# Optimization experiments

Hardware: AMD Instinct MI355X
Metric: run time of the kernel (lower is better)

Reference implementation:

```python
import jax, jax.numpy as jnp
import numpy as np

N = 100000       # num nodes
E = 3200000      # num edges (avg degree 32)
F_IN = 128       # num_node_features
HID = 16         # hidden dim hard-coded in Net
C = 10           # num_classes


def setup_inputs() -> dict:
    key = jax.random.key(0)
    k1, k2, k3, k4 = jax.random.split(key, 4)
    x = jax.random.normal(k1, (N, F_IN), dtype=jnp.float32)
    edge_index = jax.random.randint(k2, (2, E), 0, N, dtype=jnp.int32)
    W1 = jax.random.normal(k3, (F_IN, HID), dtype=jnp.float32) * 0.05
    b1 = jnp.zeros((HID,), dtype=jnp.float32)
    W2 = jax.random.normal(k4, (HID, C), dtype=jnp.float32) * 0.05
    b2 = jnp.zeros((C,), dtype=jnp.float32)
    return {"x": x, "edge_index": edge_index, "W1": W1, "b1": b1, "W2": W2, "b2": b2}


def reference(x, edge_index, W1, b1, W2, b2):
    # GCNConv: out = D^{-1/2} (A + I) D^{-1/2} X W + b   (add self-loops)
    loops = jnp.arange(N, dtype=edge_index.dtype)
    row = jnp.concatenate([edge_index[0], loops])  # source nodes
    col = jnp.concatenate([edge_index[1], loops])  # target nodes

    # symmetric normalization (degrees include self-loops, so deg >= 1)
    deg = jax.ops.segment_sum(jnp.ones_like(col, dtype=jnp.float32), col, num_segments=N)
    dis = jax.lax.rsqrt(deg)
    norm = dis[row] * dis[col]  # [E+N]

    def gcn_conv(h, W, b):
        h = h @ W                               # [N, d_out] small GEMM first
        msg = h[row] * norm[:, None]            # gather + scale, [E+N, d_out]
        out = jax.ops.segment_sum(msg, col, num_segments=N)  # scatter-add
        return out + b

    h = jax.nn.relu(gcn_conv(x, W1, b1))
    # F.dropout(training=False) is identity in eval mode
    logits = gcn_conv(h, W2, b2)
    return jax.nn.log_softmax(logits, axis=1)
```

## Files before the change

kernel.cpp:

```cpp
#include <hip/hip_runtime.h>
#include <math.h>

#define N_NODES 100000
#define N_EDGES 3200000
#define F_IN 128
#define HID 16
#define C_OUT 10
#define WIN 256
#define NDIG 391
#define PNB2 500
#define EPB 6400
#define SCN (NDIG * PNB2)
#define SB1 764
#define MAXE3 10
#define CSRLDS 10240

typedef unsigned short u16;
typedef unsigned int u32;

__device__ __forceinline__ float bf2f(u16 u) {
    return __uint_as_float(((u32)u) << 16);
}
__device__ __forceinline__ u16 f2bf(float f) {
    u32 x = __float_as_uint(f);
    u32 r = (x + 0x7fffu + ((x >> 16) & 1u)) >> 16;
    return (u16)r;
}
__device__ __forceinline__ void acc8(float* a, uint4 w) {
    a[0] += bf2f((u16)(w.x & 0xffff)); a[1] += bf2f((u16)(w.x >> 16));
    a[2] += bf2f((u16)(w.y & 0xffff)); a[3] += bf2f((u16)(w.y >> 16));
    a[4] += bf2f((u16)(w.z & 0xffff)); a[5] += bf2f((u16)(w.z >> 16));
    a[6] += bf2f((u16)(w.w & 0xffff)); a[7] += bf2f((u16)(w.w >> 16));
}

__global__ void k_pcnt(const int* __restrict__ col, int* __restrict__ blkhistA) {
    __shared__ int h[NDIG];
    for (int i = threadIdx.x; i < NDIG; i += 256) h[i] = 0;
    __syncthreads();
    const uint4* c4 = (const uint4*)(col + blockIdx.x * EPB);
    for (int i = threadIdx.x; i < EPB / 4; i += 256) {
        uint4 c = c4[i];
        atomicAdd(&h[c.x >> 8], 1);
        atomicAdd(&h[c.y >> 8], 1);
        atomicAdd(&h[c.z >> 8], 1);
        atomicAdd(&h[c.w >> 8], 1);
    }
    __syncthreads();
    for (int d = threadIdx.x; d < NDIG; d += 256)
        blkhistA[d * PNB2 + blockIdx.x] = h[d];
}

__global__ void k_s1(const int* __restrict__ blkhistA, int* __restrict__ psum) {
    __shared__ int sm[256];
    int i = blockIdx.x * 256 + threadIdx.x;
    sm[threadIdx.x] = (i < SCN) ? blkhistA[i] : 0;
    __syncthreads();
    for (int off = 128; off > 0; off >>= 1) {
        if (threadIdx.x < off) sm[threadIdx.x] += sm[threadIdx.x + off];
        __syncthreads();
    }
    if (threadIdx.x == 0) psum[blockIdx.x] = sm[0];
}

__global__ void k_s3(const int* __restrict__ blkhistA, const int* __restrict__ psum,
                     int* __restrict__ blkhistB) {
    __shared__ int ps[1024];
    __shared__ int sm[256];
    int t = threadIdx.x;
    for (int i = t; i < 1024; i += 256) ps[i] = (i < SB1) ? psum[i] : 0;
    __syncthreads();
    for (int off = 1; off < 1024; off <<= 1) {
        int v[4];
#pragma unroll
        for (int j = 0; j < 4; j++) {
            int idx = t + j * 256;
            v[j] = ps[idx] + ((idx >= off) ? ps[idx - off] : 0);
        }
        __syncthreads();
#pragma unroll
        for (int j = 0; j < 4; j++) ps[t + j * 256] = v[j];
        __syncthreads();
    }
    int bpre = (blockIdx.x > 0) ? ps[blockIdx.x - 1] : 0;

    int i = blockIdx.x * 256 + t;
    int v = (i < SCN) ? blkhistA[i] : 0;
    sm[t] = v;
    __syncthreads();
    for (int off = 1; off < 256; off <<= 1) {
        int a = sm[t];
        int b = (t >= off) ? sm[t - off] : 0;
        __syncthreads();
        sm[t] = a + b;
        __syncthreads();
    }
    if (i < SCN) blkhistB[i] = bpre + sm[t] - v;
}

__global__ void __launch_bounds__(512) k_pwrite(
        const int* __restrict__ row, const int* __restrict__ col,
        const int* __restrict__ blkhistA, const int* __restrict__ blkhistB,
        u32* __restrict__ staging) {
    __shared__ u32 sorted[EPB];
    __shared__ u16 dwin[EPB];
    __shared__ int gbase[NDIG];
    __shared__ int lbase[NDIG];
    __shared__ int lcur[NDIG];
    __shared__ int scan[512];

    int t = threadIdx.x;
    int b = blockIdx.x;
    int hv = 0;
    if (t < NDIG) {
        hv = blkhistA[t * PNB2 + b];
        gbase[t] = blkhistB[t * PNB2 + b];
        lcur[t] = 0;
    }
    scan[t] = hv;
    __syncthreads();
    for (int off = 1; off < 512; off <<= 1) {
        int v = scan[t];
        int u = (t >= off) ? scan[t - off] : 0;
        __syncthreads();
        scan[t] = v + u;
        __syncthreads();
    }
    if (t < NDIG) lbase[t] = scan[t] - hv;
    __syncthreads();

    const uint4* c4 = (const uint4*)(col + b * EPB);
    const uint4* r4 = (const uint4*)(row + b * EPB);
    for (int i = t; i < EPB / 4; i += 512) {
        uint4 c = c4[i];
        uint4 r = r4[i];
        int d, rank, pos;
        d = (int)(c.x >> 8); rank = atomicAdd(&lcur[d], 1); pos = lbase[d] + rank;
        sorted[pos] = ((c.x & 255u) << 17) | r.x; dwin[pos] = (u16)d;
        d = (int)(c.y >> 8); rank = atomicAdd(&lcur[d], 1); pos = lbase[d] + rank;
        sorted[pos] = ((c.y & 255u) << 17) | r.y; dwin[pos] = (u16)d;
        d = (int)(c.z >> 8); rank = atomicAdd(&lcur[d], 1); pos = lbase[d] + rank;
        sorted[pos] = ((c.z & 255u) << 17) | r.z; dwin[pos] = (u16)d;
        d = (int)(c.w >> 8); rank = atomicAdd(&lcur[d], 1); pos = lbase[d] + rank;
        sorted[pos] = ((c.w & 255u) << 17) | r.w; dwin[pos] = (u16)d;
    }
    __syncthreads();

    for (int i = t; i < EPB; i += 512) {
        int d = dwin[i];
        staging[gbase[d] + (i - lbase[d])] = sorted[i];
    }
}

__global__ void __launch_bounds__(256) k_gemm1d(
        const float* __restrict__ x, const float* __restrict__ W1,
        const u32* __restrict__ staging, const int* __restrict__ blkhistB,
        float* __restrict__ dis, u16* __restrict__ h1s) {
    __shared__ float Ws[F_IN * HID];
    __shared__ int cnt[WIN];
    int w = blockIdx.x;
    int t = threadIdx.x;
    for (int i = t; i < F_IN * HID; i += 256) Ws[i] = W1[i];
    cnt[t] = 0;
    __syncthreads();
    int start = blkhistB[w * PNB2];
    int end = (w == NDIG - 1) ? N_EDGES : blkhistB[(w + 1) * PNB2];
    for (int i = start + t; i < end; i += 256)
        atomicAdd(&cnt[staging[i] >> 17], 1);
    __syncthreads();

    int node = w * WIN + t;
    if (node >= N_NODES) return;
    float d = rsqrtf(1.0f + (float)cnt[t]);
    dis[node] = d;

    float acc[HID];
#pragma unroll
    for (int j = 0; j < HID; j++) acc[j] = 0.f;

    const float4* xr = (const float4*)(x + (size_t)node * F_IN);
#pragma unroll 2
    for (int k4 = 0; k4 < F_IN / 4; k4++) {
        float4 v = xr[k4];
        float xv[4] = {v.x, v.y, v.z, v.w};
#pragma unroll
        for (int kk = 0; kk < 4; kk++) {
            const float4* wr = (const float4*)(Ws + (k4 * 4 + kk) * HID);
            float4 w0 = wr[0], w1 = wr[1], w2 = wr[2], w3 = wr[3];
            float xs = xv[kk];
            acc[0]  += xs * w0.x; acc[1]  += xs * w0.y; acc[2]  += xs * w0.z; acc[3]  += xs * w0.w;
            acc[4]  += xs * w1.x; acc[5]  += xs * w1.y; acc[6]  += xs * w1.z; acc[7]  += xs * w1.w;
            acc[8]  += xs * w2.x; acc[9]  += xs * w2.y; acc[10] += xs * w2.z; acc[11] += xs * w2.w;
            acc[12] += xs * w3.x; acc[13] += xs * w3.y; acc[14] += xs * w3.z; acc[15] += xs * w3.w;
        }
    }

    u32 p[8];
#pragma unroll
    for (int i = 0; i < 8; i++)
        p[i] = (u32)f2bf(acc[2 * i] * d) | ((u32)f2bf(acc[2 * i + 1] * d) << 16);
    u32* dst = (u32*)(h1s + (size_t)node * HID);
#pragma unroll
    for (int i = 0; i < 8; i++) dst[i] = p[i];
}

__global__ void __launch_bounds__(1024) k_gl1f(
        u32* staging, const int* __restrict__ blkhistB,
        const u16* __restrict__ h1s, const float* __restrict__ b1,
        const float* __restrict__ W2,
        int* __restrict__ offs, u16* __restrict__ h2s) {
    __shared__ u32 sorted[CSRLDS];
    __shared__ int cnt[WIN];
    __shared__ int sbase[WIN];
    __shared__ int cur[WIN];
    __shared__ float Ws[HID * C_OUT];
    __shared__ float b1s[HID];
    int w = blockIdx.x;
    int t = threadIdx.x;
    if (t < HID * C_OUT) Ws[t] = W2[t];
    if (t < HID) b1s[t] = b1[t];
    if (t < WIN) cnt[t] = 0;
    __syncthreads();
    int start = blkhistB[w * PNB2];
    int end = (w == NDIG - 1) ? N_EDGES : blkhistB[(w + 1) * PNB2];
    int m = end - start;
    u32 buf[MAXE3];
    int n = 0;
#pragma unroll
    for (int k = 0; k < MAXE3; k++) {
        int i = k * 1024 + t;
        if (i < m) {
            u32 e = staging[start + i];
            buf[k] = e;
            n = k + 1;
            atomicAdd(&cnt[e >> 17], 1);
        }
    }
    __syncthreads();
    if (t < WIN) sbase[t] = cnt[t];
    __syncthreads();
    for (int off = 1; off < WIN; off <<= 1) {
        int v = 0;
        if (t < WIN) {
            v = sbase[t];
            if (t >= off) v += sbase[t - off];
        }
        __syncthreads();
        if (t < WIN) sbase[t] = v;
        __syncthreads();
    }
    if (t < WIN) {
        int excl = sbase[t] - cnt[t];
        sbase[t] = excl;
        cur[t] = excl;
        int node = w * WIN + t;
        if (node < N_NODES) offs[node] = start + excl;
    }
    if (w == 0 && t == 0) offs[N_NODES] = N_EDGES;
    __syncthreads();
#pragma unroll
    for (int k = 0; k < MAXE3; k++) {
        if (k < n) {
            u32 e = buf[k];
            int pos = atomicAdd(&cur[(int)(e >> 17)], 1);
            sorted[pos] = e;
        }
    }
    __syncthreads();
    for (int i = t; i < m; i += 1024)
        staging[start + i] = sorted[i];

    const uint4* hb = (const uint4*)h1s;
    int half = (t >> 2) & 1;
    int eq = t & 3;
#pragma unroll 1
    for (int rep = 0; rep < 2; rep++) {
        int nl = rep * 128 + (t >> 3);
        int node = w * WIN + nl;
        bool valid = node < N_NODES;
        float a[8] = {0.f, 0.f, 0.f, 0.f, 0.f, 0.f, 0.f, 0.f};
        int deg = valid ? cnt[nl] : 0;
        int s0 = sbase[nl];
        if (valid && eq == 0) acc8(a, hb[(size_t)node * 2 + half]);
        int lo = s0 + ((deg * eq) >> 2);
        int hi = s0 + ((deg * (eq + 1)) >> 2);
        int j = lo;
        for (; j + 4 <= hi; j += 4) {
            u32 e0 = sorted[j], e1 = sorted[j + 1], e2 = sorted[j + 2], e3 = sorted[j + 3];
            uint4 w0 = hb[(size_t)(e0 & 0x1FFFFu) * 2 + half];
            uint4 w1 = hb[(size_t)(e1 & 0x1FFFFu) * 2 + half];
            uint4 w2 = hb[(size_t)(e2 & 0x1FFFFu) * 2 + half];
            uint4 w3 = hb[(size_t)(e3 & 0x1FFFFu) * 2 + half];
            acc8(a, w0); acc8(a, w1); acc8(a, w2); acc8(a, w3);
        }
        for (; j < hi; j++)
            acc8(a, hb[(size_t)(sorted[j] & 0x1FFFFu) * 2 + half]);

#pragma unroll
        for (int k = 0; k < 8; k++) {
            a[k] += __shfl_xor(a[k], 1);
            a[k] += __shfl_xor(a[k], 2);
        }

        float dc = rsqrtf(1.0f + (float)deg);
        float own[8], oth[8];
#pragma unroll
        for (int k = 0; k < 8; k++) own[k] = a[k] * dc;
#pragma unroll
        for (int k = 0; k < 8; k++) oth[k] = __shfl_xor(own[k], 4);
        float h[16];
#pragma unroll
        for (int k = 0; k < 8; k++) {
            h[k]     = half ? oth[k] : own[k];
            h[8 + k] = half ? own[k] : oth[k];
        }
#pragma unroll
        for (int jj = 0; jj < 16; jj++) h[jj] = fmaxf(h[jj] + b1s[jj], 0.f);

        int nf = half ? 2 : 8;
        float outv[8];
#pragma unroll
        for (int k = 0; k < 8; k++) {
            float s = 0.f;
            if (k < nf) {
                int kk = half * 8 + k;
#pragma unroll
                for (int jj = 0; jj < 16; jj++) s += h[jj] * Ws[jj * C_OUT + kk];
            }
            outv[k] = s * dc;
        }
        if (valid && eq == 0) {
            uint4 ov;
            ov.x = (u32)f2bf(outv[0]) | ((u32)f2bf(outv[1]) << 16);
            ov.y = half ? 0u : ((u32)f2bf(outv[2]) | ((u32)f2bf(outv[3]) << 16));
            ov.z = half ? 0u : ((u32)f2bf(outv[4]) | ((u32)f2bf(outv[5]) << 16));
            ov.w = half ? 0u : ((u32)f2bf(outv[6]) | ((u32)f2bf(outv[7]) << 16));
            ((uint4*)h2s)[(size_t)node * 2 + half] = ov;
        }
    }
}

__global__ void k_gather2(const int* __restrict__ offs, const u32* __restrict__ csr,
                          const float* __restrict__ dis, const u16* __restrict__ h2s,
                          const float* __restrict__ b2, float* __restrict__ out) {
    __shared__ float b2s[C_OUT];
    if (threadIdx.x < C_OUT) b2s[threadIdx.x] = b2[threadIdx.x];
    __syncthreads();

    int t = blockIdx.x * 256 + threadIdx.x;
    if (t >= N_NODES * 8) return;
    int node = t >> 3;
    int q = t & 7;
    int half = q >> 2;
    int eq = q & 3;
    const uint4* hb = (const uint4*)h2s;
    float a[8] = {0.f, 0.f, 0.f, 0.f, 0.f, 0.f, 0.f, 0.f};
    if (eq == 0) acc8(a, hb[(size_t)node * 2 + half]);
    int o = offs[node + half];
    int oo = __shfl_xor(o, 4);
    int s0 = half ? oo : o;
    int s1 = half ? o : oo;
    int len = s1 - s0;
    int lo = s0 + ((len * eq) >> 2);
    int hi = s0 + ((len * (eq + 1)) >> 2);
    int j = lo;
    for (; j < hi && (j & 3); j++)
        acc8(a, hb[(size_t)(csr[j] & 0x1FFFFu) * 2 + half]);
    for (; j + 8 <= hi; j += 8) {
        uint4 sa = *(const uint4*)(csr + j);
        uint4 sb = *(const uint4*)(csr + j + 4);
        uint4 w0 = hb[(size_t)(sa.x & 0x1FFFFu) * 2 + half];
        uint4 w1 = hb[(size_t)(sa.y & 0x1FFFFu) * 2 + half];
        uint4 w2 = hb[(size_t)(sa.z & 0x1FFFFu) * 2 + half];
        uint4 w3 = hb[(size_t)(sa.w & 0x1FFFFu) * 2 + half];
        uint4 w4 = hb[(size_t)(sb.x & 0x1FFFFu) * 2 + half];
        uint4 w5 = hb[(size_t)(sb.y & 0x1FFFFu) * 2 + half];
        uint4 w6 = hb[(size_t)(sb.z & 0x1FFFFu) * 2 + half];
        uint4 w7 = hb[(size_t)(sb.w & 0x1FFFFu) * 2 + half];
        acc8(a, w0); acc8(a, w1); acc8(a, w2); acc8(a, w3);
        acc8(a, w4); acc8(a, w5); acc8(a, w6); acc8(a, w7);
    }
    for (; j + 4 <= hi; j += 4) {
        uint4 ss = *(const uint4*)(csr + j);
        uint4 w0 = hb[(size_t)(ss.x & 0x1FFFFu) * 2 + half];
        uint4 w1 = hb[(size_t)(ss.y & 0x1FFFFu) * 2 + half];
        uint4 w2 = hb[(size_t)(ss.z & 0x1FFFFu) * 2 + half];
        uint4 w3 = hb[(size_t)(ss.w & 0x1FFFFu) * 2 + half];
        acc8(a, w0); acc8(a, w1); acc8(a, w2); acc8(a, w3);
    }
    for (; j < hi; j++)
        acc8(a, hb[(size_t)(csr[j] & 0x1FFFFu) * 2 + half]);

#pragma unroll
    for (int k = 0; k < 8; k++) {
        a[k] += __shfl_xor(a[k], 1);
        a[k] += __shfl_xor(a[k], 2);
    }

    float dc = dis[node];
    int nf = half ? 2 : 8;
    float lg[8];
    float m = -1e30f;
#pragma unroll
    for (int k = 0; k < 8; k++) {
        lg[k] = a[k] * dc + b2s[(half * 8 + k) % C_OUT];
        if (k < nf) m = fmaxf(m, lg[k]);
    }
    m = fmaxf(m, __shfl_xor(m, 4));
    float s = 0.f;
#pragma unroll
    for (int k = 0; k < 8; k++)
        if (k < nf) s += expf(lg[k] - m);
    s += __shfl_xor(s, 4);
    float ls = logf(s) + m;
    if (eq == 0) {
        float* dst = out + (size_t)node * C_OUT + half * 8;
        if (half == 0) {
#pragma unroll
            for (int i = 0; i < 4; i++)
                *(float2*)(dst + 2 * i) = make_float2(lg[2 * i] - ls, lg[2 * i + 1] - ls);
        } else {
            *(float2*)dst = make_float2(lg[0] - ls, lg[1] - ls);
        }
    }
}

extern "C" void kernel_launch(void* const* d_in, const int* in_sizes, int n_in,
                              void* d_out, int out_size, void* d_ws, size_t ws_size,
                              hipStream_t stream) {
    const float* x  = (const float*)d_in[0];
    const int*   ei = (const int*)d_in[1];
    const float* W1 = (const float*)d_in[2];
    const float* b1 = (const float*)d_in[3];
    const float* W2 = (const float*)d_in[4];
    const float* b2 = (const float*)d_in[5];
    float* out = (float*)d_out;

    const int* row = ei;
    const int* col = ei + N_EDGES;

    char* ws = (char*)d_ws;
    float* dis      = (float*)(ws);
    int*   offs     = (int*)(ws + 400000);
    int*   blkhistA = (int*)(ws + 800016);
    int*   blkhistB = (int*)(ws + 1582352);
    int*   psum     = (int*)(ws + 2364688);
    u32*   staging  = (u32*)(ws + 2367744);
    u16*   h1s      = (u16*)(ws + 15167744);
    u16*   h2s      = (u16*)(ws + 18367744);

    const int B = 256;
    int gN8 = (N_NODES * 8 + B - 1) / B;

    k_pcnt  <<<PNB2, B, 0, stream>>>(col, blkhistA);
    k_s1    <<<SB1, B, 0, stream>>>(blkhistA, psum);
    k_s3    <<<SB1, B, 0, stream>>>(blkhistA, psum, blkhistB);
    k_pwrite<<<PNB2, 512, 0, stream>>>(row, col, blkhistA, blkhistB, staging);
    k_gemm1d<<<NDIG, B, 0, stream>>>(x, W1, staging, blkhistB, dis, h1s);
    k_gl1f  <<<NDIG, 1024, 0, stream>>>(staging, blkhistB, h1s, b1, W2, offs, h2s);
    k_gather2<<<gN8, B, 0, stream>>>(offs, staging, dis, h2s, b2, out);
}
```

Measured before the change: 218.4 us.

## Split layer-2 features into 8+2 arrays, vectorize degree count, shrink gl1f blocks

Layer-2 bf16 features move from a padded 32-byte row into two arrays: 8 features as uint4 and the last 2 features as one u32. The upper-half lanes of the final gather therefore fetch 4 bytes per edge instead of 16, which cuts gather traffic. The degree count in the first GEMM kernel now reads the staging buffer as uint4 with head and tail handling. The fused layer-1 kernel drops from 1024 to 512 threads per block, using twice as many registers per thread for edge buffering and twice as many row passes. The new 8+2 split leads to divergent branches within each 8-lane group.

```diff
diff --git a/kernel.cpp b/kernel.cpp
--- a/kernel.cpp
+++ b/kernel.cpp
@@ -12,7 +12,7 @@
 #define EPB 6400
 #define SCN (NDIG * PNB2)
 #define SB1 764
-#define MAXE3 10
+#define MAXE2 20
 #define CSRLDS 10240
 
 typedef unsigned short u16;
@@ -164,8 +164,21 @@
     __syncthreads();
     int start = blkhistB[w * PNB2];
     int end = (w == NDIG - 1) ? N_EDGES : blkhistB[(w + 1) * PNB2];
-    for (int i = start + t; i < end; i += 256)
-        atomicAdd(&cnt[staging[i] >> 17], 1);
+    int head = (4 - (start & 3)) & 3;
+    if (head > end - start) head = end - start;
+    if (t < head) atomicAdd(&cnt[staging[start + t] >> 17], 1);
+    int abody = start + head;
+    int nb = (end - abody) >> 2;
+    const uint4* s4 = (const uint4*)(staging + abody);
+    for (int i = t; i < nb; i += 256) {
+        uint4 e = s4[i];
+        atomicAdd(&cnt[e.x >> 17], 1);
+        atomicAdd(&cnt[e.y >> 17], 1);
+        atomicAdd(&cnt[e.z >> 17], 1);
+        atomicAdd(&cnt[e.w >> 17], 1);
+    }
+    int tstart = abody + (nb << 2);
+    if (t < end - tstart) atomicAdd(&cnt[staging[tstart + t] >> 17], 1);
     __syncthreads();
 
     int node = w * WIN + t;
@@ -203,11 +216,11 @@
     for (int i = 0; i < 8; i++) dst[i] = p[i];
 }
 
-__global__ void __launch_bounds__(1024) k_gl1f(
+__global__ void __launch_bounds__(512) k_gl1f(
         u32* staging, const int* __restrict__ blkhistB,
         const u16* __restrict__ h1s, const float* __restrict__ b1,
         const float* __restrict__ W2,
-        int* __restrict__ offs, u16* __restrict__ h2s) {
+        int* __restrict__ offs, uint4* __restrict__ h2a, u32* __restrict__ h2b) {
     __shared__ u32 sorted[CSRLDS];
     __shared__ int cnt[WIN];
     __shared__ int sbase[WIN];
@@ -223,11 +236,11 @@
     int start = blkhistB[w * PNB2];
     int end = (w == NDIG - 1) ? N_EDGES : blkhistB[(w + 1) * PNB2];
     int m = end - start;
-    u32 buf[MAXE3];
+    u32 buf[MAXE2];
     int n = 0;
 #pragma unroll
-    for (int k = 0; k < MAXE3; k++) {
-        int i = k * 1024 + t;
+    for (int k = 0; k < MAXE2; k++) {
+        int i = k * 512 + t;
         if (i < m) {
             u32 e = staging[start + i];
             buf[k] = e;
@@ -258,7 +271,7 @@
     if (w == 0 && t == 0) offs[N_NODES] = N_EDGES;
     __syncthreads();
 #pragma unroll
-    for (int k = 0; k < MAXE3; k++) {
+    for (int k = 0; k < MAXE2; k++) {
         if (k < n) {
             u32 e = buf[k];
             int pos = atomicAdd(&cur[(int)(e >> 17)], 1);
@@ -266,15 +279,15 @@
         }
     }
     __syncthreads();
-    for (int i = t; i < m; i += 1024)
+    for (int i = t; i < m; i += 512)
         staging[start + i] = sorted[i];
 
     const uint4* hb = (const uint4*)h1s;
     int half = (t >> 2) & 1;
     int eq = t & 3;
 #pragma unroll 1
-    for (int rep = 0; rep < 2; rep++) {
-        int nl = rep * 128 + (t >> 3);
+    for (int rep = 0; rep < 4; rep++) {
+        int nl = rep * 64 + (t >> 3);
         int node = w * WIN + nl;
         bool valid = node < N_NODES;
         float a[8] = {0.f, 0.f, 0.f, 0.f, 0.f, 0.f, 0.f, 0.f};
@@ -329,18 +342,23 @@
             outv[k] = s * dc;
         }
         if (valid && eq == 0) {
-            uint4 ov;
-            ov.x = (u32)f2bf(outv[0]) | ((u32)f2bf(outv[1]) << 16);
-            ov.y = half ? 0u : ((u32)f2bf(outv[2]) | ((u32)f2bf(outv[3]) << 16));
-            ov.z = half ? 0u : ((u32)f2bf(outv[4]) | ((u32)f2bf(outv[5]) << 16));
-            ov.w = half ? 0u : ((u32)f2bf(outv[6]) | ((u32)f2bf(outv[7]) << 16));
-            ((uint4*)h2s)[(size_t)node * 2 + half] = ov;
+            if (half == 0) {
+                uint4 ov;
+                ov.x = (u32)f2bf(outv[0]) | ((u32)f2bf(outv[1]) << 16);
+                ov.y = (u32)f2bf(outv[2]) | ((u32)f2bf(outv[3]) << 16);
+                ov.z = (u32)f2bf(outv[4]) | ((u32)f2bf(outv[5]) << 16);
+                ov.w = (u32)f2bf(outv[6]) | ((u32)f2bf(outv[7]) << 16);
+                h2a[node] = ov;
+            } else {
+                h2b[node] = (u32)f2bf(outv[0]) | ((u32)f2bf(outv[1]) << 16);
+            }
         }
     }
 }
 
 __global__ void k_gather2(const int* __restrict__ offs, const u32* __restrict__ csr,
-                          const float* __restrict__ dis, const u16* __restrict__ h2s,
+                          const float* __restrict__ dis, const uint4* __restrict__ h2a,
+                          const u32* __restrict__ h2b,
                           const float* __restrict__ b2, float* __restrict__ out) {
     __shared__ float b2s[C_OUT];
     if (threadIdx.x < C_OUT) b2s[threadIdx.x] = b2[threadIdx.x];
@@ -352,9 +370,16 @@
     int q = t & 7;
     int half = q >> 2;
     int eq = q & 3;
-    const uint4* hb = (const uint4*)h2s;
     float a[8] = {0.f, 0.f, 0.f, 0.f, 0.f, 0.f, 0.f, 0.f};
-    if (eq == 0) acc8(a, hb[(size_t)node * 2 + half]);
+    if (eq == 0) {
+        if (half == 0) {
+            acc8(a, h2a[node]);
+        } else {
+            u32 sc = h2b[node];
+            a[0] += bf2f((u16)(sc & 0xffff));
+            a[1] += bf2f((u16)(sc >> 16));
+        }
+    }
     int o = offs[node + half];
     int oo = __shfl_xor(o, 4);
     int s0 = half ? oo : o;
@@ -363,32 +388,44 @@
     int lo = s0 + ((len * eq) >> 2);
     int hi = s0 + ((len * (eq + 1)) >> 2);
     int j = lo;
-    for (; j < hi && (j & 3); j++)
-        acc8(a, hb[(size_t)(csr[j] & 0x1FFFFu) * 2 + half]);
-    for (; j + 8 <= hi; j += 8) {
-        uint4 sa = *(const uint4*)(csr + j);
-        uint4 sb = *(const uint4*)(csr + j + 4);
-        uint4 w0 = hb[(size_t)(sa.x & 0x1FFFFu) * 2 + half];
-        uint4 w1 = hb[(size_t)(sa.y & 0x1FFFFu) * 2 + half];
-        uint4 w2 = hb[(size_t)(sa.z & 0x1FFFFu) * 2 + half];
-        uint4 w3 = hb[(size_t)(sa.w & 0x1FFFFu) * 2 + half];
-        uint4 w4 = hb[(size_t)(sb.x & 0x1FFFFu) * 2 + half];
-        uint4 w5 = hb[(size_t)(sb.y & 0x1FFFFu) * 2 + half];
-        uint4 w6 = hb[(size_t)(sb.z & 0x1FFFFu) * 2 + half];
-        uint4 w7 = hb[(size_t)(sb.w & 0x1FFFFu) * 2 + half];
-        acc8(a, w0); acc8(a, w1); acc8(a, w2); acc8(a, w3);
-        acc8(a, w4); acc8(a, w5); acc8(a, w6); acc8(a, w7);
+    for (; j < hi && (j & 3); j++) {
+        u32 src = csr[j] & 0x1FFFFu;
+        if (half == 0) {
+            acc8(a, h2a[src]);
+        } else {
+            u32 v = h2b[src];
+            a[0] += bf2f((u16)(v & 0xffff));
+            a[1] += bf2f((u16)(v >> 16));
+        }
     }
     for (; j + 4 <= hi; j += 4) {
         uint4 ss = *(const uint4*)(csr + j);
-        uint4 w0 = hb[(size_t)(ss.x & 0x1FFFFu) * 2 + half];
-        uint4 w1 = hb[(size_t)(ss.y & 0x1FFFFu) * 2 + half];
-        uint4 w2 = hb[(size_t)(ss.z & 0x1FFFFu) * 2 + half];
-        uint4 w3 = hb[(size_t)(ss.w & 0x1FFFFu) * 2 + half];
-        acc8(a, w0); acc8(a, w1); acc8(a, w2); acc8(a, w3);
-    }
-    for (; j < hi; j++)
-        acc8(a, hb[(size_t)(csr[j] & 0x1FFFFu) * 2 + half]);
+        u32 i0 = ss.x & 0x1FFFFu, i1 = ss.y & 0x1FFFFu;
+        u32 i2 = ss.z & 0x1FFFFu, i3 = ss.w & 0x1FFFFu;
+        if (half == 0) {
+            uint4 w0 = h2a[i0];
+            uint4 w1 = h2a[i1];
+            uint4 w2 = h2a[i2];
+            uint4 w3 = h2a[i3];
+            acc8(a, w0); acc8(a, w1); acc8(a, w2); acc8(a, w3);
+        } else {
+            u32 v0 = h2b[i0], v1 = h2b[i1], v2 = h2b[i2], v3 = h2b[i3];
+            a[0] += bf2f((u16)(v0 & 0xffff)); a[1] += bf2f((u16)(v0 >> 16));
+            a[0] += bf2f((u16)(v1 & 0xffff)); a[1] += bf2f((u16)(v1 >> 16));
+            a[0] += bf2f((u16)(v2 & 0xffff)); a[1] += bf2f((u16)(v2 >> 16));
+            a[0] += bf2f((u16)(v3 & 0xffff)); a[1] += bf2f((u16)(v3 >> 16));
+        }
+    }
+    for (; j < hi; j++) {
+        u32 src = csr[j] & 0x1FFFFu;
+        if (half == 0) {
+            acc8(a, h2a[src]);
+        } else {
+            u32 v = h2b[src];
+            a[0] += bf2f((u16)(v & 0xffff));
+            a[1] += bf2f((u16)(v >> 16));
+        }
+    }
 
 #pragma unroll
     for (int k = 0; k < 8; k++) {
@@ -398,12 +435,15 @@
 
     float dc = dis[node];
     int nf = half ? 2 : 8;
+    int fb = half * 8;
     float lg[8];
     float m = -1e30f;
 #pragma unroll
     for (int k = 0; k < 8; k++) {
-        lg[k] = a[k] * dc + b2s[(half * 8 + k) % C_OUT];
-        if (k < nf) m = fmaxf(m, lg[k]);
+        if (k < nf) {
+            lg[k] = a[k] * dc + b2s[fb + k];
+            m = fmaxf(m, lg[k]);
+        }
     }
     m = fmaxf(m, __shfl_xor(m, 4));
     float s = 0.f;
@@ -446,7 +486,8 @@
     int*   psum     = (int*)(ws + 2364688);
     u32*   staging  = (u32*)(ws + 2367744);
     u16*   h1s      = (u16*)(ws + 15167744);
-    u16*   h2s      = (u16*)(ws + 18367744);
+    uint4* h2a      = (uint4*)(ws + 18367744);
+    u32*   h2b      = (u32*)(ws + 19967744);
 
     const int B = 256;
     int gN8 = (N_NODES * 8 + B - 1) / B;
@@ -456,6 +497,6 @@
     k_s3    <<<SB1, B, 0, stream>>>(blkhistA, psum, blkhistB);
     k_pwrite<<<PNB2, 512, 0, stream>>>(row, col, blkhistA, blkhistB, staging);
     k_gemm1d<<<NDIG, B, 0, stream>>>(x, W1, staging, blkhistB, dis, h1s);
-    k_gl1f  <<<NDIG, 1024, 0, stream>>>(staging, blkhistB, h1s, b1, W2, offs, h2s);
-    k_gather2<<<gN8, B, 0, stream>>>(offs, staging, dis, h2s, b2, out);
-}
+    k_gl1f  <<<NDIG, 512, 0, stream>>>(staging, blkhistB, h1s, b1, W2, offs, h2a, h2b);
+    k_gather2<<<gN8, B, 0, stream>>>(offs, staging, dis, h2a, h2b, b2, out);
+}
```

Result: faster. 213.8 us (-2.1%).
